# Kernel optimization log

Hardware: AMD Instinct MI355X
Metric: run time of the kernel (lower is better)

Reference implementation:

```python
import jax, jax.numpy as jnp
import numpy as np

B, D, H, C, HALT_H, MAX_STEPS = 8192, 2048, 1024, 1000, 32, 10
EPS = 1e-08


def setup_inputs() -> dict:
    key = jax.random.key(0)
    ks = jax.random.split(key, 12)
    s = 0.02
    return {
        "x": jax.random.normal(ks[0], (B, D), jnp.float32),
        "enc_W": jax.random.normal(ks[1], (H, D), jnp.float32) * s,
        "enc_b": jnp.zeros((H,), jnp.float32),
        "ln_g": jnp.ones((H,), jnp.float32),
        "ln_b": jnp.zeros((H,), jnp.float32),
        "W_ih": jax.random.normal(ks[2], (3 * H, H), jnp.float32) * s,
        "W_hh": jax.random.normal(ks[3], (3 * H, H), jnp.float32) * s,
        "b_ih": jnp.zeros((3 * H,), jnp.float32),
        "b_hh": jnp.zeros((3 * H,), jnp.float32),
        "cls_W": jax.random.normal(ks[4], (C, H), jnp.float32) * s,
        "cls_b": jnp.zeros((C,), jnp.float32),
        "h1_W": jax.random.normal(ks[5], (HALT_H, H), jnp.float32) * s,
        "h1_b": jnp.zeros((HALT_H,), jnp.float32),
        "h2_W": jax.random.normal(ks[6], (1, HALT_H), jnp.float32) * s,
        "h2_b": jnp.zeros((1,), jnp.float32),
    }


def _forward(x, enc_W, enc_b, ln_g, ln_b, W_ih, W_hh, b_ih, b_hh,
             cls_W, cls_b, h1_W, h1_b, h2_W, h2_b):
    # encoder: Linear -> LayerNorm -> GELU (exact)
    z = x @ enc_W.T + enc_b
    mu = jnp.mean(z, axis=-1, keepdims=True)
    var = jnp.var(z, axis=-1, keepdims=True)
    z = (z - mu) * jax.lax.rsqrt(var + 1e-05) * ln_g + ln_b
    h0 = jax.nn.gelu(z, approximate=False)

    def step(h, _):
        gi = h @ W_ih.T + b_ih   # GRUCell with input = hidden
        gh = h @ W_hh.T + b_hh
        gi_r, gi_z, gi_n = jnp.split(gi, 3, axis=-1)
        gh_r, gh_z, gh_n = jnp.split(gh, 3, axis=-1)
        r = jax.nn.sigmoid(gi_r + gh_r)
        zt = jax.nn.sigmoid(gi_z + gh_z)
        n = jnp.tanh(gi_n + r * gh_n)
        h_new = (1.0 - zt) * n + zt * h
        logits = h_new @ cls_W.T + cls_b                         # [B, C]
        halt = jax.nn.sigmoid(
            jax.nn.relu(h_new @ h1_W.T + h1_b) @ h2_W.T + h2_b
        )[:, 0]                                                   # [B]
        return h_new, (logits, halt)

    _, (logits_steps, halt_steps) = jax.lax.scan(step, h0, None, length=MAX_STEPS)
    logits_stack = jnp.transpose(logits_steps, (1, 0, 2))  # [B, T, C]
    halts_stack = jnp.transpose(halt_steps, (1, 0))        # [B, T]

    log_not_halt = jnp.log(1.0 - halts_stack + EPS)
    cumsum_log = jnp.cumsum(log_not_halt, axis=1)
    cumsum_shifted = jnp.concatenate(
        [jnp.zeros((halts_stack.shape[0], 1), halts_stack.dtype), cumsum_log[:, :-1]], axis=1)
    halt_dist = halts_stack * jnp.exp(cumsum_shifted)
    remainder = 1.0 - jnp.sum(halt_dist, axis=1, keepdims=True)
    halt_dist = jnp.concatenate(
        [halt_dist[:, :-1], halt_dist[:, -1:] + jnp.maximum(remainder, 0.0)], axis=1)

    weighted_logits = jnp.sum(halt_dist[:, :, None] * logits_stack, axis=1)  # [B, C]
    step_indices = jnp.arange(1, MAX_STEPS + 1, dtype=weighted_logits.dtype)
    expected_steps = jnp.sum(halt_dist * step_indices, axis=1)
    probs = jax.nn.softmax(weighted_logits, axis=1)
    softmax_conf = jnp.max(probs, axis=1)
    comp_uncertainty = expected_steps / MAX_STEPS
    confidence = 0.7 * softmax_conf + 0.3 * (1.0 - comp_uncertainty)
    return (weighted_logits, probs, confidence, softmax_conf,
            expected_steps, halt_dist, comp_uncertainty)


def reference(x, enc_W, enc_b, ln_g, ln_b, W_ih, W_hh, b_ih, b_hh,
              cls_W, cls_b, h1_W, h1_b, h2_W, h2_b):
    return _forward(x, enc_W, enc_b, ln_g, ln_b, W_ih, W_hh, b_ih, b_hh,
                    cls_W, cls_b, h1_W, h1_b, h2_W, h2_b)
```

## Files before the change

kernel.cpp:

```cpp
#include <hip/hip_runtime.h>
#include <hip/hip_bf16.h>

#define B_ 8192
#define D_ 2048
#define H_ 1024
#define C_ 1000
#define NSTEP 10

typedef __attribute__((ext_vector_type(8))) short short8;
typedef __attribute__((ext_vector_type(4))) float f32x4;

__device__ __forceinline__ f32x4 mfma16x16(short8 a, short8 b, f32x4 c) {
  return __builtin_amdgcn_mfma_f32_16x16x32_bf16(a, b, c, 0, 0, 0);
}

__device__ __forceinline__ void async16(void* lds_uniform, const void* gsrc) {
  __builtin_amdgcn_global_load_lds(
      (const __attribute__((address_space(1))) void*)gsrc,
      (__attribute__((address_space(3))) void*)lds_uniform, 16, 0, 0);
}

__device__ __forceinline__ float sigm(float x) { return 1.0f / (1.0f + __expf(-x)); }
__device__ __forceinline__ float tanh_fast(float x) { return 1.0f - 2.0f / (__expf(2.0f * x) + 1.0f); }
__device__ __forceinline__ float b2f(short s) {
  union { unsigned u; float f; } v; v.u = ((unsigned)(unsigned short)s) << 16; return v.f;
}
__device__ __forceinline__ unsigned short f2us(float f) {
  __hip_bfloat16 h = __float2bfloat16(f); return *(unsigned short*)&h;
}

__device__ __forceinline__ int swz(int row, int slot) {
  return (row << 7) + (((slot) ^ (row & 7)) << 4);
}

__global__ void cvt_bf16_pad(const float* __restrict__ src, __hip_bfloat16* __restrict__ dst,
                             int n4, int nsrc4) {
  int i = blockIdx.x * 256 + threadIdx.x;
  if (i >= n4) return;
  float4 v = make_float4(0.f, 0.f, 0.f, 0.f);
  if (i < nsrc4) v = ((const float4*)src)[i];
  ((ushort4*)dst)[i] = make_ushort4(f2us(v.x), f2us(v.y), f2us(v.z), f2us(v.w));
}

__global__ void cvt_gates(const float* __restrict__ Wih, const float* __restrict__ Whh,
                          __hip_bfloat16* __restrict__ dst) {
  const int i = blockIdx.x * 256 + threadIdx.x;
  const int per_gate = (H_ * H_) / 4;
  const int gate = i / per_gate, rem = i - gate * per_gate;
  float4 v;
  if (gate == 0) {
    float4 a = ((const float4*)Wih)[rem], b = ((const float4*)Whh)[rem];
    v = make_float4(a.x + b.x, a.y + b.y, a.z + b.z, a.w + b.w);
  } else if (gate == 1) {
    float4 a = ((const float4*)Wih)[per_gate + rem], b = ((const float4*)Whh)[per_gate + rem];
    v = make_float4(a.x + b.x, a.y + b.y, a.z + b.z, a.w + b.w);
  } else if (gate == 2) {
    v = ((const float4*)Wih)[2 * per_gate + rem];
  } else {
    v = ((const float4*)Whh)[2 * per_gate + rem];
  }
  ((ushort4*)dst)[i] = make_ushort4(f2us(v.x), f2us(v.y), f2us(v.z), f2us(v.w));
}

template<int EPI>
__global__ __launch_bounds__(256, 2)
void gemm_bt(const __hip_bfloat16* __restrict__ A, int lda,
             const __hip_bfloat16* __restrict__ Bt, int ldb, int K,
             const float* __restrict__ bias,
             float* __restrict__ out, int out_ld, int ncol,
             const float* __restrict__ wrow) {
  __shared__ __hip_bfloat16 sA[128 * 64];
  __shared__ __hip_bfloat16 sB[128 * 64];
  const int tid = threadIdx.x;
  const int wave = tid >> 6, lane = tid & 63;
  const int m0 = blockIdx.x * 128, n0 = blockIdx.y * 128;
  const int wm = (wave >> 1) * 64, wn = (wave & 1) * 64;
  const int lr = lane & 15;
  const int g4 = lane >> 4;
  const int srow = wave * 8 + (lane >> 3);
  const int scol = ((lane & 7) ^ ((lane >> 3) & 7)) * 8;

  f32x4 acc[4][4] = {};

  const __hip_bfloat16* Asrc = A + (size_t)(m0 + srow) * lda + scol;
  const __hip_bfloat16* Bsrc = Bt + (size_t)(n0 + srow) * ldb + scol;

  for (int k0 = 0; k0 < K; k0 += 64) {
#pragma unroll
    for (int c = 0; c < 4; ++c) {
      async16((char*)sA + c * 4096 + wave * 1024, Asrc + (size_t)(c * 32) * lda + k0);
      async16((char*)sB + c * 4096 + wave * 1024, Bsrc + (size_t)(c * 32) * ldb + k0);
    }
    __syncthreads();
#pragma unroll
    for (int ks = 0; ks < 2; ++ks) {
      const int slot = ks * 4 + g4;
      short8 af[4], bfr[4];
#pragma unroll
      for (int i = 0; i < 4; ++i) {
        af[i]  = *(const short8*)((const char*)sA + swz(wm + i * 16 + lr, slot));
        bfr[i] = *(const short8*)((const char*)sB + swz(wn + i * 16 + lr, slot));
      }
#pragma unroll
      for (int i = 0; i < 4; ++i)
#pragma unroll
        for (int j = 0; j < 4; ++j)
          acc[i][j] = mfma16x16(af[i], bfr[j], acc[i][j]);
    }
    __syncthreads();
  }

  const int rbase = (lane >> 4) * 4;
  const int cbase = lane & 15;
#pragma unroll
  for (int i = 0; i < 4; ++i) {
#pragma unroll
    for (int r = 0; r < 4; ++r) {
      const int grow = m0 + wm + i * 16 + rbase + r;
      if (EPI == 1) {
        const float ws = wrow[grow];
#pragma unroll
        for (int j = 0; j < 4; ++j) {
          const int gcol = n0 + wn + j * 16 + cbase;
          if (gcol < ncol)
            out[(size_t)grow * out_ld + gcol] = acc[i][j][r] + bias[gcol] * ws;
        }
      } else {
#pragma unroll
        for (int j = 0; j < 4; ++j) {
          const int gcol = n0 + wn + j * 16 + cbase;
          out[(size_t)grow * out_ld + gcol] = acc[i][j][r] + bias[gcol];
        }
      }
    }
  }
}

__global__ __launch_bounds__(256, 2)
void gemm_gru(const __hip_bfloat16* __restrict__ A,
              const __hip_bfloat16* __restrict__ Wc4,
              const float* __restrict__ b_ih, const float* __restrict__ b_hh,
              __hip_bfloat16* __restrict__ hnewb) {
  __shared__ __hip_bfloat16 sA[128 * 64];
  __shared__ __hip_bfloat16 sB[4 * 32 * 64];
  const int tid = threadIdx.x, wave = tid >> 6, lane = tid & 63;
  const int m0 = blockIdx.x * 128, n0 = blockIdx.y * 32;
  const int wr = wave >> 1, wc = wave & 1;
  const int lr = lane & 15;
  const int g4 = lane >> 4;
  const int srow = lane >> 3;
  const int scol = ((lane & 7) ^ ((lane >> 3) & 7)) * 8;

  f32x4 acc[4][4] = {};

  const __hip_bfloat16* Asrc = A + (size_t)(m0 + wave * 8 + srow) * H_ + scol;
  const __hip_bfloat16* Bsrc = Wc4 + (size_t)(n0 + wave * 8 + srow) * H_ + scol;

  for (int k0 = 0; k0 < H_; k0 += 64) {
#pragma unroll
    for (int c = 0; c < 4; ++c)
      async16((char*)sA + c * 4096 + wave * 1024, Asrc + (size_t)(c * 32) * H_ + k0);
#pragma unroll
    for (int g = 0; g < 4; ++g)
      async16((char*)sB + g * 4096 + wave * 1024, Bsrc + ((size_t)g << 20) + k0);
    __syncthreads();
#pragma unroll
    for (int ks = 0; ks < 2; ++ks) {
      const int slot = ks * 4 + g4;
      short8 af[4];
#pragma unroll
      for (int mi = 0; mi < 4; ++mi)
        af[mi] = *(const short8*)((const char*)sA + swz(wr * 64 + mi * 16 + lr, slot));
      short8 bf[4];
#pragma unroll
      for (int g = 0; g < 4; ++g)
        bf[g] = *(const short8*)((const char*)sB + g * 4096 + swz(wc * 16 + lr, slot));
#pragma unroll
      for (int mi = 0; mi < 4; ++mi)
#pragma unroll
        for (int g = 0; g < 4; ++g)
          acc[mi][g] = mfma16x16(af[mi], bf[g], acc[mi][g]);
    }
    __syncthreads();
  }

  const int rbase = (lane >> 4) * 4;
  const int cbase = lane & 15;
  const int gcol = n0 + wc * 16 + cbase;
  const float brz = b_ih[gcol] + b_hh[gcol];
  const float bzz = b_ih[H_ + gcol] + b_hh[H_ + gcol];
  const float bin = b_ih[2 * H_ + gcol];
  const float bhn = b_hh[2 * H_ + gcol];
#pragma unroll
  for (int mi = 0; mi < 4; ++mi) {
#pragma unroll
    for (int r = 0; r < 4; ++r) {
      const int grow = m0 + wr * 64 + mi * 16 + rbase + r;
      const size_t idx = (size_t)grow * H_ + gcol;
      const float rg = sigm(acc[mi][0][r] + brz);
      const float zg = sigm(acc[mi][1][r] + bzz);
      const float ng = tanh_fast(acc[mi][2][r] + bin + rg * (acc[mi][3][r] + bhn));
      const float hv = b2f(*(const short*)(A + idx));
      hnewb[idx] = __float2bfloat16((1.0f - zg) * ng + zg * hv);
    }
  }
}

__global__ void ln_gelu(const float* __restrict__ z, const float* __restrict__ g,
                        const float* __restrict__ bta, __hip_bfloat16* __restrict__ hb) {
  const int row = blockIdx.x, t = threadIdx.x;
  __shared__ float rs[4], rs2[4];
  float4 v = ((const float4*)(z + (size_t)row * H_))[t];
  float s = v.x + v.y + v.z + v.w;
  float s2 = v.x * v.x + v.y * v.y + v.z * v.z + v.w * v.w;
#pragma unroll
  for (int off = 32; off; off >>= 1) {
    s += __shfl_down(s, off);
    s2 += __shfl_down(s2, off);
  }
  if ((t & 63) == 0) { rs[t >> 6] = s; rs2[t >> 6] = s2; }
  __syncthreads();
  const float mu = (rs[0] + rs[1] + rs[2] + rs[3]) * (1.0f / H_);
  const float var = (rs2[0] + rs2[1] + rs2[2] + rs2[3]) * (1.0f / H_) - mu * mu;
  const float rstd = rsqrtf(var + 1e-5f);
  float4 gg = ((const float4*)g)[t];
  float4 bb = ((const float4*)bta)[t];
  float o[4], res[4];
  o[0] = (v.x - mu) * rstd * gg.x + bb.x;
  o[1] = (v.y - mu) * rstd * gg.y + bb.y;
  o[2] = (v.z - mu) * rstd * gg.z + bb.z;
  o[3] = (v.w - mu) * rstd * gg.w + bb.w;
#pragma unroll
  for (int k = 0; k < 4; ++k)
    res[k] = 0.5f * o[k] * (1.0f + erff(o[k] * 0.70710678118654752f));
  ((ushort4*)(hb + (size_t)row * H_))[t] =
      make_ushort4(f2us(res[0]), f2us(res[1]), f2us(res[2]), f2us(res[3]));
}

__global__ __launch_bounds__(256, 4)
void halt_mlp_all(const __hip_bfloat16* __restrict__ hstack,
                  const __hip_bfloat16* __restrict__ h1Wb,
                  const float* __restrict__ h1b, const float* __restrict__ h2W,
                  const float* __restrict__ h2b,
                  float* __restrict__ hbuf) {
  __shared__ float part[2][2][64][8];
  const int tid = threadIdx.x, wave = tid >> 6, lane = tid & 63;
  const int tstep = blockIdx.y;
  const __hip_bfloat16* hb = hstack + (size_t)(tstep + 1) * B_ * H_;
  const int rowgrp = wave >> 1, khalf = wave & 1;
  const int m0 = (blockIdx.x * 2 + rowgrp) * 16;
  const int lr = lane & 15, lk = (lane >> 4) * 8;

  const __hip_bfloat16* Arow = hb + (size_t)(m0 + lr) * H_ + khalf * 512 + lk;
  const __hip_bfloat16* B0 = h1Wb + (size_t)lr * H_ + khalf * 512 + lk;
  const __hip_bfloat16* B1 = h1Wb + (size_t)(16 + lr) * H_ + khalf * 512 + lk;
  f32x4 acc0 = {}, acc1 = {};
#pragma unroll 4
  for (int kk = 0; kk < 512; kk += 32) {
    short8 a  = *(const short8*)(Arow + kk);
    short8 b0 = *(const short8*)(B0 + kk);
    short8 b1 = *(const short8*)(B1 + kk);
    acc0 = mfma16x16(a, b0, acc0);
    acc1 = mfma16x16(a, b1, acc1);
  }
#pragma unroll
  for (int q = 0; q < 4; ++q) {
    part[rowgrp][khalf][lane][q]     = acc0[q];
    part[rowgrp][khalf][lane][4 + q] = acc1[q];
  }
  __syncthreads();
  if (khalf) return;

  const float w2a = h2W[lr], w2b = h2W[16 + lr];
  const float b1a = h1b[lr], b1b = h1b[16 + lr];
  float p[4];
#pragma unroll
  for (int q = 0; q < 4; ++q) {
    const float u0 = part[rowgrp][0][lane][q]     + part[rowgrp][1][lane][q]     + b1a;
    const float u1 = part[rowgrp][0][lane][4 + q] + part[rowgrp][1][lane][4 + q] + b1b;
    p[q] = fmaxf(u0, 0.f) * w2a + fmaxf(u1, 0.f) * w2b;
  }
#pragma unroll
  for (int m = 1; m < 16; m <<= 1) {
#pragma unroll
    for (int q = 0; q < 4; ++q) p[q] += __shfl_xor(p[q], m);
  }
  if (lr == 0) {
    const float b2 = h2b[0];
#pragma unroll
    for (int q = 0; q < 4; ++q) {
      const int row = m0 + (lane >> 4) * 4 + q;
      hbuf[(size_t)row * NSTEP + tstep] = 1.f / (1.f + expf(-(p[q] + b2)));
    }
  }
}

__global__ void ponder_rec(const float* __restrict__ hbuf,
                           float* __restrict__ out_hd, float* __restrict__ out_es,
                           float* __restrict__ out_cu, float* __restrict__ wsum) {
  const int row = blockIdx.x * 256 + threadIdx.x;
  const float* hp = hbuf + (size_t)row * NSTEP;
  float c = 0.f, ps = 0.f, es = 0.f;
  float hd[NSTEP];
#pragma unroll
  for (int t = 0; t < NSTEP; ++t) {
    const float halt = hp[t];
    const float pt = halt * expf(c);
    float w;
    if (t == NSTEP - 1) {
      w = pt + fmaxf(1.f - (ps + pt), 0.f);
    } else {
      w = pt;
      c += logf(1.f - halt + 1e-8f);
      ps += pt;
    }
    es += w * (float)(t + 1);
    hd[t] = w;
  }
#pragma unroll
  for (int t = 0; t < NSTEP; ++t) out_hd[(size_t)row * NSTEP + t] = hd[t];
  out_es[row] = es;
  out_cu[row] = es * (1.0f / NSTEP);
  wsum[row] = ps + hd[NSTEP - 1];
}

__global__ void hw_final(const __hip_bfloat16* __restrict__ hstack,
                         const float* __restrict__ out_hd,
                         __hip_bfloat16* __restrict__ hwb) {
  const int t = threadIdx.x;
  const int row = blockIdx.x * 4 + (t >> 6);
  const int c0 = (t & 63) * 16;
  const float* hd = out_hd + (size_t)row * NSTEP;
  float accv[16] = {};
#pragma unroll
  for (int s = 0; s < NSTEP; ++s) {
    const float w = hd[s];
    const short8* p = (const short8*)(hstack + ((size_t)(s + 1) * B_ + row) * H_ + c0);
    short8 a0 = p[0], a1 = p[1];
#pragma unroll
    for (int q = 0; q < 8; ++q) accv[q] += w * b2f(a0[q]);
#pragma unroll
    for (int q = 0; q < 8; ++q) accv[8 + q] += w * b2f(a1[q]);
  }
  short8 r0, r1;
#pragma unroll
  for (int q = 0; q < 8; ++q) { r0[q] = (short)f2us(accv[q]); r1[q] = (short)f2us(accv[8 + q]); }
  short8* dst = (short8*)(hwb + (size_t)row * H_ + c0);
  dst[0] = r0; dst[1] = r1;
}

__global__ void finalize(const float* __restrict__ wl, const float* __restrict__ es,
                         float* __restrict__ probs, float* __restrict__ conf,
                         float* __restrict__ sconf) {
  const int row = blockIdx.x, t = threadIdx.x;
  __shared__ float red[4], red2[4];
  float4 v = make_float4(-1e30f, -1e30f, -1e30f, -1e30f);
  float m = -1e30f;
  if (t < 250) {
    v = ((const float4*)(wl + (size_t)row * C_))[t];
    m = fmaxf(fmaxf(v.x, v.y), fmaxf(v.z, v.w));
  }
#pragma unroll
  for (int off = 32; off; off >>= 1) m = fmaxf(m, __shfl_down(m, off));
  if ((t & 63) == 0) red[t >> 6] = m;
  __syncthreads();
  m = fmaxf(fmaxf(red[0], red[1]), fmaxf(red[2], red[3]));
  float4 e = make_float4(0.f, 0.f, 0.f, 0.f);
  float s = 0.f;
  if (t < 250) {
    e.x = expf(v.x - m); e.y = expf(v.y - m); e.z = expf(v.z - m); e.w = expf(v.w - m);
    s = e.x + e.y + e.z + e.w;
  }
#pragma unroll
  for (int off = 32; off; off >>= 1) s += __shfl_down(s, off);
  if ((t & 63) == 0) red2[t >> 6] = s;
  __syncthreads();
  s = red2[0] + red2[1] + red2[2] + red2[3];
  const float inv = 1.0f / s;
  if (t < 250)
    ((float4*)(probs + (size_t)row * C_))[t] = make_float4(e.x * inv, e.y * inv, e.z * inv, e.w * inv);
  if (t == 0) {
    sconf[row] = inv;
    conf[row] = 0.7f * inv + 0.3f * (1.0f - es[row] * (1.0f / NSTEP));
  }
}

extern "C" void kernel_launch(void* const* d_in, const int* in_sizes, int n_in,
                              void* d_out, int out_size, void* d_ws, size_t ws_size,
                              hipStream_t stream) {
  (void)in_sizes; (void)n_in; (void)out_size; (void)ws_size;
  const float* x     = (const float*)d_in[0];
  const float* enc_W = (const float*)d_in[1];
  const float* enc_b = (const float*)d_in[2];
  const float* ln_g  = (const float*)d_in[3];
  const float* ln_b  = (const float*)d_in[4];
  const float* W_ih  = (const float*)d_in[5];
  const float* W_hh  = (const float*)d_in[6];
  const float* b_ih  = (const float*)d_in[7];
  const float* b_hh  = (const float*)d_in[8];
  const float* cls_W = (const float*)d_in[9];
  const float* cls_b = (const float*)d_in[10];
  const float* h1_W  = (const float*)d_in[11];
  const float* h1_b  = (const float*)d_in[12];
  const float* h2_W  = (const float*)d_in[13];
  const float* h2_b  = (const float*)d_in[14];

  char* wsp = (char*)d_ws;
  auto carve = [&](size_t n) { char* p = wsp; wsp += (n + 255) & ~(size_t)255; return p; };
  __hip_bfloat16* Wc4b   = (__hip_bfloat16*)carve((size_t)4 * H_ * H_ * 2);
  __hip_bfloat16* clsWb  = (__hip_bfloat16*)carve((size_t)1024 * 1024 * 2);
  __hip_bfloat16* encWb  = (__hip_bfloat16*)carve((size_t)H_ * D_ * 2);
  __hip_bfloat16* h1Wb   = (__hip_bfloat16*)carve((size_t)32 * H_ * 2);
  __hip_bfloat16* hstack = (__hip_bfloat16*)carve((size_t)(NSTEP + 1) * B_ * H_ * 2);
  float* wsum = (float*)carve((size_t)B_ * 4);
  float* hbuf = (float*)carve((size_t)B_ * NSTEP * 4);

  const size_t SLOT = (size_t)B_ * H_;
  float* z            = (float*)(hstack + SLOT);
  __hip_bfloat16* xb  = hstack + 3 * SLOT;
  __hip_bfloat16* hwb = hstack;

  float* out = (float*)d_out;
  float* out_wl    = out;
  float* out_probs = out + (size_t)B_ * C_;
  float* out_conf  = out + (size_t)2 * B_ * C_;
  float* out_sconf = out_conf + B_;
  float* out_es    = out_sconf + B_;
  float* out_hd    = out_es + B_;
  float* out_cu    = out_hd + (size_t)B_ * NSTEP;

  dim3 blk(256);
  { int n4 = B_ * D_ / 4;       cvt_bf16_pad<<<(n4 + 255) / 256, blk, 0, stream>>>(x, xb, n4, n4); }
  { int n4 = H_ * D_ / 4;       cvt_bf16_pad<<<(n4 + 255) / 256, blk, 0, stream>>>(enc_W, encWb, n4, n4); }
  { int n4 = 4 * H_ * H_ / 4;   cvt_gates<<<(n4 + 255) / 256, blk, 0, stream>>>(W_ih, W_hh, Wc4b); }
  { int n4 = 1024 * 1024 / 4;   cvt_bf16_pad<<<(n4 + 255) / 256, blk, 0, stream>>>(cls_W, clsWb, n4, C_ * H_ / 4); }
  { int n4 = 32 * H_ / 4;       cvt_bf16_pad<<<(n4 + 255) / 256, blk, 0, stream>>>(h1_W, h1Wb, n4, n4); }

  gemm_bt<0><<<dim3(B_ / 128, H_ / 128), blk, 0, stream>>>(
      xb, D_, encWb, D_, D_, enc_b, z, H_, H_, nullptr);
  ln_gelu<<<B_, blk, 0, stream>>>(z, ln_g, ln_b, hstack);

  for (int step = 0; step < NSTEP; ++step) {
    const __hip_bfloat16* hprev = hstack + (size_t)step * SLOT;
    __hip_bfloat16* hnext = hstack + (size_t)(step + 1) * SLOT;
    gemm_gru<<<dim3(B_ / 128, H_ / 32), blk, 0, stream>>>(
        hprev, Wc4b, b_ih, b_hh, hnext);
  }

  halt_mlp_all<<<dim3(B_ / 32, NSTEP), blk, 0, stream>>>(
      hstack, h1Wb, h1_b, h2_W, h2_b, hbuf);
  ponder_rec<<<B_ / 256, blk, 0, stream>>>(hbuf, out_hd, out_es, out_cu, wsum);

  hw_final<<<B_ / 4, blk, 0, stream>>>(hstack, out_hd, hwb);

  gemm_bt<1><<<dim3(B_ / 128, 1024 / 128), blk, 0, stream>>>(
      hwb, H_, clsWb, H_, H_, cls_b, out_wl, C_, C_, wsum);

  finalize<<<B_, blk, 0, stream>>>(out_wl, out_es, out_probs, out_conf, out_sconf);
}
```

Before: 936.5 us.

## Widen GRU GEMM tile to 64 columns and use 32x32x16 MFMA

The fused GRU step GEMM now computes a 128x64 hidden-column tile (times four gate blocks) per workgroup instead of 128x32, using 32x32x16 bf16 MFMA instructions in place of 16x16x32. This halves the grid along N, increases reuse of each loaded A tile across more weight columns, and cuts LDS fragment reads per MFMA. The epilogue is remapped to the 32x32 accumulator layout. Cost: the B LDS buffer doubles, raising shared memory per block and possibly lowering occupancy, and the grid has fewer blocks.

Measured after the change: 1.012 ms. +8.1%, slower.

```diff
diff --git a/kernel.cpp b/kernel.cpp
--- a/kernel.cpp
+++ b/kernel.cpp
@@ -9,9 +9,13 @@
 
 typedef __attribute__((ext_vector_type(8))) short short8;
 typedef __attribute__((ext_vector_type(4))) float f32x4;
+typedef __attribute__((ext_vector_type(16))) float f32x16;
 
 __device__ __forceinline__ f32x4 mfma16x16(short8 a, short8 b, f32x4 c) {
   return __builtin_amdgcn_mfma_f32_16x16x32_bf16(a, b, c, 0, 0, 0);
+}
+__device__ __forceinline__ f32x16 mfma32x32(short8 a, short8 b, f32x16 c) {
+  return __builtin_amdgcn_mfma_f32_32x32x16_bf16(a, b, c, 0, 0, 0);
 }
 
 __device__ __forceinline__ void async16(void* lds_uniform, const void* gsrc) {
@@ -142,19 +146,19 @@
               const float* __restrict__ b_ih, const float* __restrict__ b_hh,
               __hip_bfloat16* __restrict__ hnewb) {
   __shared__ __hip_bfloat16 sA[128 * 64];
-  __shared__ __hip_bfloat16 sB[4 * 32 * 64];
+  __shared__ __hip_bfloat16 sB[4 * 64 * 64];
   const int tid = threadIdx.x, wave = tid >> 6, lane = tid & 63;
-  const int m0 = blockIdx.x * 128, n0 = blockIdx.y * 32;
+  const int m0 = blockIdx.x * 128, n0 = blockIdx.y * 64;
   const int wr = wave >> 1, wc = wave & 1;
-  const int lr = lane & 15;
-  const int g4 = lane >> 4;
-  const int srow = lane >> 3;
+  const int wm = wr * 64;
+  const int l31 = lane & 31;
+  const int kg = lane >> 5;
   const int scol = ((lane & 7) ^ ((lane >> 3) & 7)) * 8;
 
-  f32x4 acc[4][4] = {};
-
-  const __hip_bfloat16* Asrc = A + (size_t)(m0 + wave * 8 + srow) * H_ + scol;
-  const __hip_bfloat16* Bsrc = Wc4 + (size_t)(n0 + wave * 8 + srow) * H_ + scol;
+  f32x16 acc[2][4] = {};
+
+  const __hip_bfloat16* Asrc = A + (size_t)(m0 + (tid >> 3)) * H_ + scol;
+  const __hip_bfloat16* Bsrc = Wc4 + (size_t)(n0 + (tid >> 3)) * H_ + scol;
 
   for (int k0 = 0; k0 < H_; k0 += 64) {
 #pragma unroll
@@ -162,44 +166,44 @@
       async16((char*)sA + c * 4096 + wave * 1024, Asrc + (size_t)(c * 32) * H_ + k0);
 #pragma unroll
     for (int g = 0; g < 4; ++g)
-      async16((char*)sB + g * 4096 + wave * 1024, Bsrc + ((size_t)g << 20) + k0);
+#pragma unroll
+      for (int d = 0; d < 2; ++d)
+        async16((char*)sB + g * 8192 + d * 4096 + wave * 1024,
+                Bsrc + ((size_t)g << 20) + (size_t)(d * 32) * H_ + k0);
     __syncthreads();
 #pragma unroll
-    for (int ks = 0; ks < 2; ++ks) {
-      const int slot = ks * 4 + g4;
-      short8 af[4];
-#pragma unroll
-      for (int mi = 0; mi < 4; ++mi)
-        af[mi] = *(const short8*)((const char*)sA + swz(wr * 64 + mi * 16 + lr, slot));
+    for (int ks = 0; ks < 4; ++ks) {
+      const int slot = 2 * ks + kg;
+      short8 af0 = *(const short8*)((const char*)sA + swz(wm + l31, slot));
+      short8 af1 = *(const short8*)((const char*)sA + swz(wm + 32 + l31, slot));
       short8 bf[4];
 #pragma unroll
       for (int g = 0; g < 4; ++g)
-        bf[g] = *(const short8*)((const char*)sB + g * 4096 + swz(wc * 16 + lr, slot));
-#pragma unroll
-      for (int mi = 0; mi < 4; ++mi)
-#pragma unroll
-        for (int g = 0; g < 4; ++g)
-          acc[mi][g] = mfma16x16(af[mi], bf[g], acc[mi][g]);
+        bf[g] = *(const short8*)((const char*)sB + g * 8192 + swz(wc * 32 + l31, slot));
+#pragma unroll
+      for (int g = 0; g < 4; ++g) {
+        acc[0][g] = mfma32x32(af0, bf[g], acc[0][g]);
+        acc[1][g] = mfma32x32(af1, bf[g], acc[1][g]);
+      }
     }
     __syncthreads();
   }
 
-  const int rbase = (lane >> 4) * 4;
-  const int cbase = lane & 15;
-  const int gcol = n0 + wc * 16 + cbase;
+  const int gcol = n0 + wc * 32 + l31;
   const float brz = b_ih[gcol] + b_hh[gcol];
   const float bzz = b_ih[H_ + gcol] + b_hh[H_ + gcol];
   const float bin = b_ih[2 * H_ + gcol];
   const float bhn = b_hh[2 * H_ + gcol];
-#pragma unroll
-  for (int mi = 0; mi < 4; ++mi) {
-#pragma unroll
-    for (int r = 0; r < 4; ++r) {
-      const int grow = m0 + wr * 64 + mi * 16 + rbase + r;
+  const int rb4 = 4 * kg;
+#pragma unroll
+  for (int mi = 0; mi < 2; ++mi) {
+#pragma unroll
+    for (int reg = 0; reg < 16; ++reg) {
+      const int grow = m0 + wm + mi * 32 + (reg & 3) + 8 * (reg >> 2) + rb4;
       const size_t idx = (size_t)grow * H_ + gcol;
-      const float rg = sigm(acc[mi][0][r] + brz);
-      const float zg = sigm(acc[mi][1][r] + bzz);
-      const float ng = tanh_fast(acc[mi][2][r] + bin + rg * (acc[mi][3][r] + bhn));
+      const float rg = sigm(acc[mi][0][reg] + brz);
+      const float zg = sigm(acc[mi][1][reg] + bzz);
+      const float ng = tanh_fast(acc[mi][2][reg] + bin + rg * (acc[mi][3][reg] + bhn));
       const float hv = b2f(*(const short*)(A + idx));
       hnewb[idx] = __float2bfloat16((1.0f - zg) * ng + zg * hv);
     }
@@ -443,7 +447,7 @@
   for (int step = 0; step < NSTEP; ++step) {
     const __hip_bfloat16* hprev = hstack + (size_t)step * SLOT;
     __hip_bfloat16* hnext = hstack + (size_t)(step + 1) * SLOT;
-    gemm_gru<<<dim3(B_ / 128, H_ / 32), blk, 0, stream>>>(
+    gemm_gru<<<dim3(B_ / 128, H_ / 64), blk, 0, stream>>>(
         hprev, Wc4b, b_ih, b_hh, hnext);
   }
 
```
